# Performance work log

Measured on AMD Instinct MI355X. Metric: run time of the kernel, lower is better.

The kernel has to match this reference:

```python
import jax, jax.numpy as jnp
import numpy as np

EMBED_DIM = 512
NUM_HEADS = 8
HEAD_DIM = EMBED_DIM // NUM_HEADS
NUM_TEXTS = 512
NUM_VIDS = 512
NUM_FRAMES = 12


def setup_inputs() -> dict:
    key = jax.random.key(0)
    ks = jax.random.split(key, 10)
    s = 1.0 / np.sqrt(EMBED_DIM)
    return {
        "text_embeds": jax.random.normal(ks[0], (NUM_TEXTS, EMBED_DIM), jnp.float32),
        "video_embeds": jax.random.normal(ks[1], (NUM_VIDS, NUM_FRAMES, EMBED_DIM), jnp.float32),
        "Wq": jax.random.normal(ks[2], (EMBED_DIM, EMBED_DIM), jnp.float32) * s,
        "bq": jax.random.normal(ks[3], (EMBED_DIM,), jnp.float32) * s,
        "Wk": jax.random.normal(ks[4], (EMBED_DIM, EMBED_DIM), jnp.float32) * s,
        "bk": jax.random.normal(ks[5], (EMBED_DIM,), jnp.float32) * s,
        "Wv": jax.random.normal(ks[6], (EMBED_DIM, EMBED_DIM), jnp.float32) * s,
        "bv": jax.random.normal(ks[7], (EMBED_DIM,), jnp.float32) * s,
        "Wo": jax.random.normal(ks[8], (EMBED_DIM, EMBED_DIM), jnp.float32) * s,
        "bo": jax.random.normal(ks[9], (EMBED_DIM,), jnp.float32) * s,
    }


def reference(text_embeds, video_embeds, Wq, bq, Wk, bk, Wv, bv, Wo, bo):
    T = text_embeds.shape[0]
    V, F, D = video_embeds.shape
    H, Hd = NUM_HEADS, HEAD_DIM

    # q: [T, D] -> [T, H, Hd]
    q = (text_embeds @ Wq + bq).reshape(T, H, Hd)
    # k, v: [V, F, D] -> [V, F, H, Hd]
    k = (video_embeds @ Wk + bk).reshape(V, F, H, Hd)
    v = (video_embeds @ Wv + bv).reshape(V, F, H, Hd)

    # shared-query broadcast logits: [V, H, F, T]
    logits = jnp.einsum("vfhd,thd->vhft", k, q) / np.sqrt(Hd).astype(jnp.float32)
    # softmax over frames (dim F)
    weights = jax.nn.softmax(logits, axis=2)

    # weighted sum over frames: [V, H, Hd, T] -> [V, T, D]
    attn = jnp.einsum("vfhd,vhft->vthd", v, weights).reshape(V, T, D)
    return attn @ Wo + bo
```

## Files before the change

kernel.cpp:

```cpp
#include <hip/hip_runtime.h>
#include <stdint.h>

#define T_  512
#define V_  512
#define F_  12
#define FP_ 16
#define D_  512
#define H_  8
#define HF_ 96

using half8  = __attribute__((ext_vector_type(8))) _Float16;
using f32x4  = __attribute__((ext_vector_type(4))) float;
using uint4v = __attribute__((ext_vector_type(4))) unsigned int;
using uint2v = __attribute__((ext_vector_type(2))) unsigned int;

#define OFF_TB   (0L)
#define OFF_VB   (524288L)
#define OFF_WQT  (OFF_VB  + 8388608L)
#define OFF_WKT  (OFF_WQT + 524288L)
#define OFF_WVT  (OFF_WKT + 524288L)
#define OFF_WOT  (OFF_WVT + 524288L)
#define OFF_QB   (OFF_WOT + 524288L)
#define OFF_KP   (OFF_QB  + 524288L)
#define OFF_VP   (OFF_KP  + 8388608L)
#define OFF_ZT   (OFF_VP  + 8388608L)
#define OFF_WT   (OFF_ZT  + 50331648L)

__device__ __forceinline__ unsigned short f2h(float x) {
  _Float16 h = (_Float16)x;
  return __builtin_bit_cast(unsigned short, h);
}

__device__ __forceinline__ void cvt8_store(float4 a, float4 b, unsigned short* dst) {
  unsigned int w0 = f2h(a.x) | ((unsigned int)f2h(a.y) << 16);
  unsigned int w1 = f2h(a.z) | ((unsigned int)f2h(a.w) << 16);
  unsigned int w2 = f2h(b.x) | ((unsigned int)f2h(b.y) << 16);
  unsigned int w3 = f2h(b.z) | ((unsigned int)f2h(b.w) << 16);
  uint4v v = {w0, w1, w2, w3};
  *(uint4v*)dst = v;
}

__global__ __launch_bounds__(256) void k0_prep(
    const float* __restrict__ text, const float* __restrict__ video,
    const float* __restrict__ Wq, const float* __restrict__ Wk,
    const float* __restrict__ Wv, const float* __restrict__ Wo, char* ws) {
  __shared__ unsigned short tl[64][72];
  int bx = blockIdx.x, tid = threadIdx.x;
  if (bx < 128) {
    unsigned short* tb = (unsigned short*)(ws + OFF_TB);
    long i = ((long)bx * 256 + tid) * 8;
    float4 a = *(const float4*)(text + i);
    float4 b = *(const float4*)(text + i + 4);
    cvt8_store(a, b, tb + i);
  } else if (bx < 2176) {
    unsigned short* vb = (unsigned short*)(ws + OFF_VB);
    long j = ((long)(bx - 128) * 256 + tid) * 8;
    int row = (int)(j >> 9);
    int c   = (int)(j & 511);
    int f = row & 15, v = row >> 4;
    if (f < F_) {
      const float* src = video + ((long)(v * F_ + f) << 9) + c;
      float4 a = *(const float4*)src;
      float4 b = *(const float4*)(src + 4);
      cvt8_store(a, b, vb + j);
    } else {
      uint4v z = {0, 0, 0, 0};
      *(uint4v*)(vb + j) = z;
    }
  } else {
    int tix = bx - 2176;
    int w = tix >> 6, tile = tix & 63;
    const float* W = (w == 0) ? Wq : (w == 1) ? Wk : (w == 2) ? Wv : Wo;
    unsigned short* WT = (unsigned short*)(ws +
        ((w == 0) ? OFF_WQT : (w == 1) ? OFF_WKT : (w == 2) ? OFF_WVT : OFF_WOT));
    int r0 = (tile >> 3) * 64, c0 = (tile & 7) * 64;
    int rr = tid >> 4, cc = (tid & 15) * 4;
#pragma unroll
    for (int j2 = 0; j2 < 4; ++j2) {
      int r = rr + j2 * 16;
      float4 a = *(const float4*)(W + (long)(r0 + r) * 512 + c0 + cc);
      tl[cc + 0][r] = f2h(a.x);
      tl[cc + 1][r] = f2h(a.y);
      tl[cc + 2][r] = f2h(a.z);
      tl[cc + 3][r] = f2h(a.w);
    }
    __syncthreads();
    int row_l = tid >> 2, u = (tid & 3) * 16;
    uint4v x0 = *(uint4v*)&tl[row_l][u];
    uint4v x1 = *(uint4v*)&tl[row_l][u + 8];
    unsigned short* dst = WT + (long)(c0 + row_l) * 512 + r0 + u;
    *(uint4v*)dst = x0;
    *(uint4v*)(dst + 8) = x1;
  }
}

__global__ __launch_bounds__(256) void k1_proj(
    char* ws, const float* __restrict__ bq, const float* __restrict__ bk,
    const float* __restrict__ bv) {
  __shared__ unsigned short As[128 * 72];
  __shared__ unsigned short Bs[128 * 72];
  int bx = blockIdx.x, tid = threadIdx.x;
  int nt = bx & 3, mt = bx >> 2;
  const unsigned short* A;
  const unsigned short* BT;
  const float* bias;
  float scale;
  unsigned short* out;
  int m0;
  if (mt < 4) {
    A = (const unsigned short*)(ws + OFF_TB);
    BT = (const unsigned short*)(ws + OFF_WQT);
    bias = bq; scale = 0.125f;
    out = (unsigned short*)(ws + OFF_QB);
    m0 = mt << 7;
  } else if (mt < 68) {
    A = (const unsigned short*)(ws + OFF_VB);
    BT = (const unsigned short*)(ws + OFF_WKT);
    bias = bk; scale = 1.0f;
    out = (unsigned short*)(ws + OFF_KP);
    m0 = (mt - 4) << 7;
  } else {
    A = (const unsigned short*)(ws + OFF_VB);
    BT = (const unsigned short*)(ws + OFF_WVT);
    bias = bv; scale = 1.0f;
    out = (unsigned short*)(ws + OFF_VP);
    m0 = (mt - 68) << 7;
  }
  int n0 = nt << 7;
  int lane = tid & 63, wid = tid >> 6;
  int mw = (wid >> 1) << 6, nw = (wid & 1) << 6;
  int l15 = lane & 15, g = lane >> 4;
  f32x4 acc[4][4];
#pragma unroll
  for (int i = 0; i < 4; i++)
#pragma unroll
    for (int j = 0; j < 4; j++) acc[i][j] = (f32x4){0.f, 0.f, 0.f, 0.f};

  for (int ks = 0; ks < 8; ++ks) {
    __syncthreads();
#pragma unroll
    for (int j = 0; j < 4; ++j) {
      int flat = (j * 256 + tid) * 8;
      int row = flat >> 6, col = flat & 63;
      uint4v va = *(const uint4v*)(A + (long)(m0 + row) * 512 + ks * 64 + col);
      uint4v vb = *(const uint4v*)(BT + (long)(n0 + row) * 512 + ks * 64 + col);
      *(uint4v*)(As + row * 72 + col) = va;
      *(uint4v*)(Bs + row * 72 + col) = vb;
    }
    __syncthreads();
#pragma unroll
    for (int k2 = 0; k2 < 2; ++k2) {
      half8 a[4], b[4];
#pragma unroll
      for (int i = 0; i < 4; i++) {
        a[i] = *(const half8*)(As + (mw + i * 16 + l15) * 72 + k2 * 32 + (g << 3));
        b[i] = *(const half8*)(Bs + (nw + i * 16 + l15) * 72 + k2 * 32 + (g << 3));
      }
#pragma unroll
      for (int i = 0; i < 4; i++)
#pragma unroll
        for (int j = 0; j < 4; j++)
          acc[i][j] = __builtin_amdgcn_mfma_f32_16x16x32_f16(a[i], b[j], acc[i][j], 0, 0, 0);
    }
  }
#pragma unroll
  for (int j = 0; j < 4; j++) {
    int n = n0 + nw + j * 16 + l15;
    float bsv = bias[n];
#pragma unroll
    for (int i = 0; i < 4; i++) {
      int rbase = m0 + mw + i * 16 + (g << 2);
#pragma unroll
      for (int r = 0; r < 4; r++) {
        float x = (acc[i][j][r] + bsv) * scale;
        out[(long)(rbase + r) * 512 + n] = f2h(x);
      }
    }
  }
}

__global__ __launch_bounds__(256) void k6_pz(char* ws) {
  int bx = blockIdx.x, tid = threadIdx.x;
  int lane = tid & 63, wid = tid >> 6;
  int l15 = lane & 15, g = lane >> 4;
  const unsigned short* QB = (const unsigned short*)(ws + OFF_QB);
  const unsigned short* KP = (const unsigned short*)(ws + OFF_KP);
  const unsigned short* VP = (const unsigned short*)(ws + OFF_VP);
  const unsigned short* WOT = (const unsigned short*)(ws + OFF_WOT);

  if (bx < 2048) {
    int v = bx >> 2, qt = bx & 3;
    unsigned short* Wt = (unsigned short*)(ws + OFF_WT);
    const unsigned short* kpr = KP + ((long)(v * 16 + l15) << 9);
#pragma unroll
    for (int h = 0; h < H_; ++h) {
      half8 a0 = *(const half8*)(kpr + h * 64 + (g << 3));
      half8 a1 = *(const half8*)(kpr + h * 64 + 32 + (g << 3));
#pragma unroll
      for (int ti = 0; ti < 2; ++ti) {
        int t = (qt << 7) + (wid << 5) + (ti << 4) + l15;
        const unsigned short* qr = QB + ((long)t << 9);
        half8 b0 = *(const half8*)(qr + h * 64 + (g << 3));
        half8 b1 = *(const half8*)(qr + h * 64 + 32 + (g << 3));
        f32x4 acc = {0.f, 0.f, 0.f, 0.f};
        acc = __builtin_amdgcn_mfma_f32_16x16x32_f16(a0, b0, acc, 0, 0, 0);
        acc = __builtin_amdgcn_mfma_f32_16x16x32_f16(a1, b1, acc, 0, 0, 0);
        float e0 = (g < 3) ? __expf(acc[0]) : 0.f;
        float e1 = (g < 3) ? __expf(acc[1]) : 0.f;
        float e2 = (g < 3) ? __expf(acc[2]) : 0.f;
        float e3 = (g < 3) ? __expf(acc[3]) : 0.f;
        float s = e0 + e1 + e2 + e3;
        s += __shfl_xor(s, 16);
        s += __shfl_xor(s, 32);
        float inv = 1.0f / s;
        if (g < 3) {
          unsigned int w0 = f2h(e0 * inv) | ((unsigned int)f2h(e1 * inv) << 16);
          unsigned int w1 = f2h(e2 * inv) | ((unsigned int)f2h(e3 * inv) << 16);
          uint2v pk = {w0, w1};
          *(uint2v*)(Wt + (long)(v * 512 + t) * 96 + h * 12 + (g << 2)) = pk;
        }
      }
    }
  } else {
    int b2 = bx - 2048;
    int v = b2 >> 2, qt = b2 & 3;
    unsigned short* Zt = (unsigned short*)(ws + OFF_ZT);
    const unsigned short* vpr = VP + ((long)(v * 16 + l15) << 9);
#pragma unroll
    for (int h = 0; h < H_; ++h) {
      half8 a0 = *(const half8*)(vpr + h * 64 + (g << 3));
      half8 a1 = *(const half8*)(vpr + h * 64 + 32 + (g << 3));
#pragma unroll
      for (int mf = 0; mf < 2; ++mf) {
        int n = (qt << 7) + (wid << 5) + (mf << 4) + l15;
        const unsigned short* wor = WOT + ((long)n << 9);
        half8 b0 = *(const half8*)(wor + h * 64 + (g << 3));
        half8 b1 = *(const half8*)(wor + h * 64 + 32 + (g << 3));
        f32x4 acc = {0.f, 0.f, 0.f, 0.f};
        acc = __builtin_amdgcn_mfma_f32_16x16x32_f16(a0, b0, acc, 0, 0, 0);
        acc = __builtin_amdgcn_mfma_f32_16x16x32_f16(a1, b1, acc, 0, 0, 0);
        if (g < 3) {
          unsigned int w0 = f2h(acc[0]) | ((unsigned int)f2h(acc[1]) << 16);
          unsigned int w1 = f2h(acc[2]) | ((unsigned int)f2h(acc[3]) << 16);
          uint2v pk = {w0, w1};
          *(uint2v*)(Zt + (long)(v * 512 + n) * 96 + h * 12 + (g << 2)) = pk;
        }
      }
    }
  }
}

__global__ __launch_bounds__(256, 4) void k7_gemm(char* ws, const float* __restrict__ bo,
                                                  float* __restrict__ outp) {
  int bx = blockIdx.x, tid = threadIdx.x;
  int bsw = (bx & 7) * 1024 + (bx >> 3);
  int v = bsw >> 4, tt = (bsw >> 2) & 3, nt = bsw & 3;
  const unsigned short* Wt = (const unsigned short*)(ws + OFF_WT);
  const unsigned short* Zt = (const unsigned short*)(ws + OFF_ZT);
  int lane = tid & 63, wid = tid >> 6;
  int l15 = lane & 15, g = lane >> 4;
  int mw = (wid >> 1) << 6, nw = (wid & 1) << 6;

  const unsigned short* Zb = Zt + (long)(v * 512 + (nt << 7) + nw) * 96;
  const unsigned short* Wb = Wt + (long)(v * 512 + (tt << 7) + mw) * 96;

  f32x4 acc[4][4];
#pragma unroll
  for (int i = 0; i < 4; i++)
#pragma unroll
    for (int j = 0; j < 4; j++) acc[i][j] = (f32x4){0.f, 0.f, 0.f, 0.f};

#pragma unroll
  for (int ks = 0; ks < 3; ++ks) {
    half8 zf[4], wf[4];
#pragma unroll
    for (int i = 0; i < 4; i++)
      zf[i] = *(const half8*)(Zb + (long)(i * 16 + l15) * 96 + ks * 32 + (g << 3));
#pragma unroll
    for (int j = 0; j < 4; j++)
      wf[j] = *(const half8*)(Wb + (long)(j * 16 + l15) * 96 + ks * 32 + (g << 3));
#pragma unroll
    for (int i = 0; i < 4; i++)
#pragma unroll
      for (int j = 0; j < 4; j++)
        acc[i][j] = __builtin_amdgcn_mfma_f32_16x16x32_f16(zf[i], wf[j], acc[i][j], 0, 0, 0);
  }

#pragma unroll
  for (int i = 0; i < 4; i++) {
    int n = (nt << 7) + nw + i * 16 + (g << 2);
    float4 b4 = *(const float4*)(bo + n);
#pragma unroll
    for (int j = 0; j < 4; j++) {
      int t = (tt << 7) + mw + j * 16 + l15;
      float4 o;
      o.x = acc[i][j][0] + b4.x;
      o.y = acc[i][j][1] + b4.y;
      o.z = acc[i][j][2] + b4.z;
      o.w = acc[i][j][3] + b4.w;
      *(float4*)(outp + ((long)(v * 512 + t) << 9) + n) = o;
    }
  }
}

extern "C" void kernel_launch(void* const* d_in, const int* in_sizes, int n_in,
                              void* d_out, int out_size, void* d_ws, size_t ws_size,
                              hipStream_t stream) {
  const float* text  = (const float*)d_in[0];
  const float* video = (const float*)d_in[1];
  const float* Wq = (const float*)d_in[2];
  const float* bq = (const float*)d_in[3];
  const float* Wk = (const float*)d_in[4];
  const float* bk = (const float*)d_in[5];
  const float* Wv = (const float*)d_in[6];
  const float* bv = (const float*)d_in[7];
  const float* Wo = (const float*)d_in[8];
  const float* bo = (const float*)d_in[9];
  char* ws = (char*)d_ws;
  float* out = (float*)d_out;

  k0_prep<<<dim3(2432), dim3(256), 0, stream>>>(text, video, Wq, Wk, Wv, Wo, ws);
  k1_proj<<<dim3(528), dim3(256), 0, stream>>>(ws, bq, bk, bv);
  k6_pz<<<dim3(4096), dim3(256), 0, stream>>>(ws);
  k7_gemm<<<dim3(8192), dim3(256), 0, stream>>>(ws, bo, out);
}
```

Measured before the change: 837.5 us.

## Store intermediates in MFMA-fragment-tiled layout for contiguous fragment loads

Introduces a tiled layout (16 rows by 8 fp16 columns per 128-element block) for Q, K, V projections, transposed Wo, and the Wt/Zt intermediates. Each 16-lane group's half8 fragment loads then hit one contiguous 256-byte span instead of 16 strided rows. The producer kernels (prep, projection, pz) and the consumer GEMM are all updated to use the layout. The launch_bounds occupancy hint on k7_gemm is also dropped, which may change register allocation.

```diff
diff --git a/kernel.cpp b/kernel.cpp
--- a/kernel.cpp
+++ b/kernel.cpp
@@ -25,6 +25,10 @@
 #define OFF_VP   (OFF_KP  + 8388608L)
 #define OFF_ZT   (OFF_VP  + 8388608L)
 #define OFF_WT   (OFF_ZT  + 50331648L)
+
+__device__ __forceinline__ long flh(int row, int col, int ncolg) {
+  return ((long)((row >> 4) * ncolg + (col >> 3)) << 7) + ((row & 15) << 3) + (col & 7);
+}
 
 __device__ __forceinline__ unsigned short f2h(float x) {
   _Float16 h = (_Float16)x;
@@ -88,9 +92,16 @@
     int row_l = tid >> 2, u = (tid & 3) * 16;
     uint4v x0 = *(uint4v*)&tl[row_l][u];
     uint4v x1 = *(uint4v*)&tl[row_l][u + 8];
-    unsigned short* dst = WT + (long)(c0 + row_l) * 512 + r0 + u;
-    *(uint4v*)dst = x0;
-    *(uint4v*)(dst + 8) = x1;
+    int n = c0 + row_l;
+    int d0 = r0 + u;
+    if (w == 3) {
+      *(uint4v*)(WT + flh(n, d0, 64))     = x0;
+      *(uint4v*)(WT + flh(n, d0 + 8, 64)) = x1;
+    } else {
+      unsigned short* dst = WT + (long)n * 512 + d0;
+      *(uint4v*)dst = x0;
+      *(uint4v*)(dst + 8) = x1;
+    }
   }
 }
 
@@ -173,7 +184,7 @@
 #pragma unroll
       for (int r = 0; r < 4; r++) {
         float x = (acc[i][j][r] + bsv) * scale;
-        out[(long)(rbase + r) * 512 + n] = f2h(x);
+        out[flh(rbase + r, n, 64)] = f2h(x);
       }
     }
   }
@@ -183,25 +194,24 @@
   int bx = blockIdx.x, tid = threadIdx.x;
   int lane = tid & 63, wid = tid >> 6;
   int l15 = lane & 15, g = lane >> 4;
-  const unsigned short* QB = (const unsigned short*)(ws + OFF_QB);
-  const unsigned short* KP = (const unsigned short*)(ws + OFF_KP);
-  const unsigned short* VP = (const unsigned short*)(ws + OFF_VP);
-  const unsigned short* WOT = (const unsigned short*)(ws + OFF_WOT);
+  int lo = l15 << 3;
 
   if (bx < 2048) {
     int v = bx >> 2, qt = bx & 3;
-    unsigned short* Wt = (unsigned short*)(ws + OFF_WT);
-    const unsigned short* kpr = KP + ((long)(v * 16 + l15) << 9);
+    const unsigned short* KPv = (const unsigned short*)(ws + OFF_KP) + ((long)v << 13);
+    const unsigned short* QB  = (const unsigned short*)(ws + OFF_QB);
+    unsigned short* Wtv = (unsigned short*)(ws + OFF_WT) + (long)v * 49152;
 #pragma unroll
     for (int h = 0; h < H_; ++h) {
-      half8 a0 = *(const half8*)(kpr + h * 64 + (g << 3));
-      half8 a1 = *(const half8*)(kpr + h * 64 + 32 + (g << 3));
+      half8 a0 = *(const half8*)(KPv + (((h << 3) + g) << 7) + lo);
+      half8 a1 = *(const half8*)(KPv + (((h << 3) + 4 + g) << 7) + lo);
 #pragma unroll
       for (int ti = 0; ti < 2; ++ti) {
-        int t = (qt << 7) + (wid << 5) + (ti << 4) + l15;
-        const unsigned short* qr = QB + ((long)t << 9);
-        half8 b0 = *(const half8*)(qr + h * 64 + (g << 3));
-        half8 b1 = *(const half8*)(qr + h * 64 + 32 + (g << 3));
+        int tb = (qt << 7) + (wid << 5) + (ti << 4);
+        int trg = tb >> 4;
+        const unsigned short* qrg = QB + ((long)trg << 13);
+        half8 b0 = *(const half8*)(qrg + (((h << 3) + g) << 7) + lo);
+        half8 b1 = *(const half8*)(qrg + (((h << 3) + 4 + g) << 7) + lo);
         f32x4 acc = {0.f, 0.f, 0.f, 0.f};
         acc = __builtin_amdgcn_mfma_f32_16x16x32_f16(a0, b0, acc, 0, 0, 0);
         acc = __builtin_amdgcn_mfma_f32_16x16x32_f16(a1, b1, acc, 0, 0, 0);
@@ -217,25 +227,29 @@
           unsigned int w0 = f2h(e0 * inv) | ((unsigned int)f2h(e1 * inv) << 16);
           unsigned int w1 = f2h(e2 * inv) | ((unsigned int)f2h(e3 * inv) << 16);
           uint2v pk = {w0, w1};
-          *(uint2v*)(Wt + (long)(v * 512 + t) * 96 + h * 12 + (g << 2)) = pk;
+          int k0 = h * 12 + (g << 2);
+          long ad = ((long)(trg * 12 + (k0 >> 3)) << 7) + lo + (k0 & 7);
+          *(uint2v*)(Wtv + ad) = pk;
         }
       }
     }
   } else {
     int b2 = bx - 2048;
     int v = b2 >> 2, qt = b2 & 3;
-    unsigned short* Zt = (unsigned short*)(ws + OFF_ZT);
-    const unsigned short* vpr = VP + ((long)(v * 16 + l15) << 9);
+    const unsigned short* VPv = (const unsigned short*)(ws + OFF_VP) + ((long)v << 13);
+    const unsigned short* WOT = (const unsigned short*)(ws + OFF_WOT);
+    unsigned short* Ztv = (unsigned short*)(ws + OFF_ZT) + (long)v * 49152;
 #pragma unroll
     for (int h = 0; h < H_; ++h) {
-      half8 a0 = *(const half8*)(vpr + h * 64 + (g << 3));
-      half8 a1 = *(const half8*)(vpr + h * 64 + 32 + (g << 3));
+      half8 a0 = *(const half8*)(VPv + (((h << 3) + g) << 7) + lo);
+      half8 a1 = *(const half8*)(VPv + (((h << 3) + 4 + g) << 7) + lo);
 #pragma unroll
       for (int mf = 0; mf < 2; ++mf) {
-        int n = (qt << 7) + (wid << 5) + (mf << 4) + l15;
-        const unsigned short* wor = WOT + ((long)n << 9);
-        half8 b0 = *(const half8*)(wor + h * 64 + (g << 3));
-        half8 b1 = *(const half8*)(wor + h * 64 + 32 + (g << 3));
+        int nb = (qt << 7) + (wid << 5) + (mf << 4);
+        int nrg = nb >> 4;
+        const unsigned short* wrg = WOT + ((long)nrg << 13);
+        half8 b0 = *(const half8*)(wrg + (((h << 3) + g) << 7) + lo);
+        half8 b1 = *(const half8*)(wrg + (((h << 3) + 4 + g) << 7) + lo);
         f32x4 acc = {0.f, 0.f, 0.f, 0.f};
         acc = __builtin_amdgcn_mfma_f32_16x16x32_f16(a0, b0, acc, 0, 0, 0);
         acc = __builtin_amdgcn_mfma_f32_16x16x32_f16(a1, b1, acc, 0, 0, 0);
@@ -243,26 +257,28 @@
           unsigned int w0 = f2h(acc[0]) | ((unsigned int)f2h(acc[1]) << 16);
           unsigned int w1 = f2h(acc[2]) | ((unsigned int)f2h(acc[3]) << 16);
           uint2v pk = {w0, w1};
-          *(uint2v*)(Zt + (long)(v * 512 + n) * 96 + h * 12 + (g << 2)) = pk;
+          int k0 = h * 12 + (g << 2);
+          long ad = ((long)(nrg * 12 + (k0 >> 3)) << 7) + lo + (k0 & 7);
+          *(uint2v*)(Ztv + ad) = pk;
         }
       }
     }
   }
 }
 
-__global__ __launch_bounds__(256, 4) void k7_gemm(char* ws, const float* __restrict__ bo,
-                                                  float* __restrict__ outp) {
+__global__ __launch_bounds__(256) void k7_gemm(char* ws, const float* __restrict__ bo,
+                                               float* __restrict__ outp) {
   int bx = blockIdx.x, tid = threadIdx.x;
   int bsw = (bx & 7) * 1024 + (bx >> 3);
   int v = bsw >> 4, tt = (bsw >> 2) & 3, nt = bsw & 3;
-  const unsigned short* Wt = (const unsigned short*)(ws + OFF_WT);
-  const unsigned short* Zt = (const unsigned short*)(ws + OFF_ZT);
+  const unsigned short* Wtv = (const unsigned short*)(ws + OFF_WT) + (long)v * 49152;
+  const unsigned short* Ztv = (const unsigned short*)(ws + OFF_ZT) + (long)v * 49152;
   int lane = tid & 63, wid = tid >> 6;
   int l15 = lane & 15, g = lane >> 4;
+  int lo = l15 << 3;
   int mw = (wid >> 1) << 6, nw = (wid & 1) << 6;
-
-  const unsigned short* Zb = Zt + (long)(v * 512 + (nt << 7) + nw) * 96;
-  const unsigned short* Wb = Wt + (long)(v * 512 + (tt << 7) + mw) * 96;
+  int trg0 = ((tt << 7) + mw) >> 4;
+  int nrg0 = ((nt << 7) + nw) >> 4;
 
   f32x4 acc[4][4];
 #pragma unroll
@@ -275,10 +291,10 @@
     half8 zf[4], wf[4];
 #pragma unroll
     for (int i = 0; i < 4; i++)
-      zf[i] = *(const half8*)(Zb + (long)(i * 16 + l15) * 96 + ks * 32 + (g << 3));
+      zf[i] = *(const half8*)(Ztv + ((long)((nrg0 + i) * 12 + (ks << 2) + g) << 7) + lo);
 #pragma unroll
     for (int j = 0; j < 4; j++)
-      wf[j] = *(const half8*)(Wb + (long)(j * 16 + l15) * 96 + ks * 32 + (g << 3));
+      wf[j] = *(const half8*)(Wtv + ((long)((trg0 + j) * 12 + (ks << 2) + g) << 7) + lo);
 #pragma unroll
     for (int i = 0; i < 4; i++)
 #pragma unroll
```

New measurement: 704.2 us. -15.9%, faster.
